# Kernel tuning notes

Measured on AMD Instinct MI355X. Metric: run time of the kernel, lower is better.

Reference implementation:

```python
import jax, jax.numpy as jnp
import numpy as np

EPS_MSG = 1e-7
EPS_BN = 1e-5


def _seg_softmax(logits, seg, num_segments):
    # logits: [E, D] per-edge logits; softmax over edges sharing the same dst node
    m = jax.ops.segment_max(logits, seg, num_segments=num_segments)
    m = jnp.where(jnp.isfinite(m), m, 0.0)
    e = jnp.exp(logits - m[seg])
    s = jax.ops.segment_sum(e, seg, num_segments=num_segments)
    return e / (s[seg] + 1e-16)


def _batchnorm(h, gamma, beta):
    mu = jnp.mean(h, axis=0)
    var = jnp.var(h, axis=0)
    return (h - mu) * jax.lax.rsqrt(var + EPS_BN) * gamma + beta


def setup_inputs() -> dict:
    key = jax.random.key(0)
    ks = jax.random.split(key, 12)
    N, E, G, D, L = 100000, 600000, 512, 128, 7
    x = jax.random.randint(ks[0], (N, 9), 0, 64, dtype=jnp.int32)
    edge_index = jax.random.randint(ks[1], (2, E), 0, N, dtype=jnp.int32)
    edge_attr = jax.random.randint(ks[2], (E, 3), 0, 8, dtype=jnp.int32)
    batch = jnp.sort(jax.random.randint(ks[3], (N,), 0, G, dtype=jnp.int32))
    rf_pred = jax.random.uniform(ks[4], (G,), dtype=jnp.float32)
    atom_emb = jax.random.normal(ks[5], (9, 64, D), dtype=jnp.float32) * 0.02
    bond_emb = jax.random.normal(ks[6], (3, 8, D), dtype=jnp.float32) * 0.02
    conv_w = jax.random.normal(ks[7], (L, D, D), dtype=jnp.float32) * 0.02
    conv_b = jnp.zeros((L, D), dtype=jnp.float32)
    ts = jnp.ones((L,), dtype=jnp.float32)  # learnable inverse temperatures (init 1/t style)
    gammas = jnp.ones((L, D), dtype=jnp.float32)
    bn_betas = jnp.zeros((L, D), dtype=jnp.float32)
    final_w = jax.random.normal(ks[8], (D, 1), dtype=jnp.float32) * 0.02
    final_b = jnp.zeros((1,), dtype=jnp.float32)
    beta = jnp.array([0.5], dtype=jnp.float32)
    return {"x": x, "edge_index": edge_index, "edge_attr": edge_attr, "batch": batch,
            "rf_pred": rf_pred, "atom_emb": atom_emb, "bond_emb": bond_emb,
            "conv_w": conv_w, "conv_b": conv_b, "ts": ts, "gammas": gammas,
            "bn_betas": bn_betas, "final_w": final_w, "final_b": final_b, "beta": beta}


def reference(x, edge_index, edge_attr, batch, rf_pred, atom_emb, bond_emb,
              conv_w, conv_b, ts, gammas, bn_betas, final_w, final_b, beta):
    N = x.shape[0]
    G = rf_pred.shape[0]
    L = conv_w.shape[0]
    src, dst = edge_index[0], edge_index[1]

    # AtomEncoder / BondEncoder: sum of per-feature embeddings
    h = jax.vmap(lambda tab, idx: tab[idx], in_axes=(0, 1))(atom_emb, x).sum(0)          # [N, D]
    e_emb = jax.vmap(lambda tab, idx: tab[idx], in_axes=(0, 1))(bond_emb, edge_attr).sum(0)  # [E, D]

    def genconv(l, hin):
        msg = jax.nn.relu(hin[src] + e_emb) + EPS_MSG          # [E, D]
        alpha = _seg_softmax(msg * ts[l], dst, N)              # softmax aggregation weights
        aggr = jax.ops.segment_sum(alpha * msg, dst, num_segments=N)  # [N, D]
        return (hin + aggr) @ conv_w[l] + conv_b[l]

    # res+ DeeperGCN
    h = genconv(0, h)
    for l in range(1, L):
        h2 = jax.nn.relu(_batchnorm(h, gammas[l - 1], bn_betas[l - 1]))
        h = genconv(l, h2) + h
    h = jax.nn.relu(_batchnorm(h, gammas[L - 1], bn_betas[L - 1]))

    # mean graph pooling
    counts = jnp.maximum(jax.ops.segment_sum(jnp.ones((N,), h.dtype), batch, num_segments=G), 1.0)
    hg = jax.ops.segment_sum(h, batch, num_segments=G) / counts[:, None]  # [G, D]

    dgcn_pred = hg @ final_w + final_b  # [G, 1]
    return (1.0 - beta) * jax.nn.sigmoid(dgcn_pred) + beta * rf_pred.reshape(-1, 1)
```

## Files before the change

### kernel.cpp

```cpp
#include <hip/hip_runtime.h>
#include <hip/hip_fp16.h>
#include <math.h>

#define D 128
#define PF 8

typedef _Float16 f16x8 __attribute__((ext_vector_type(8)));
typedef float f32x4_t __attribute__((ext_vector_type(4)));


__global__ void hist_kernel(const int* __restrict__ edge_index, int* __restrict__ deg, int E) {
    int e = blockIdx.x * blockDim.x + threadIdx.x;
    if (e >= E) return;
    atomicAdd(&deg[edge_index[E + e]], 1);
}

__global__ void scanA_kernel(const int* __restrict__ deg, int* __restrict__ bsum, int n) {
    __shared__ int red[256];
    int b = blockIdx.x, t = threadIdx.x;
    int base = b * 1024 + t * 4;
    int s = 0;
#pragma unroll
    for (int j = 0; j < 4; ++j)
        if (base + j < n) s += deg[base + j];
    red[t] = s;
    __syncthreads();
    for (int off = 128; off > 0; off >>= 1) {
        if (t < off) red[t] += red[t + off];
        __syncthreads();
    }
    if (t == 0) bsum[b] = red[0];
}

__global__ void scanB_kernel(int* __restrict__ bsum, int nb) {
    __shared__ int sh[256];
    int t = threadIdx.x;
    sh[t] = (t < nb) ? bsum[t] : 0;
    __syncthreads();
    for (int off = 1; off < 256; off <<= 1) {
        int v = (t >= off) ? sh[t - off] : 0;
        __syncthreads();
        sh[t] += v;
        __syncthreads();
    }
    if (t < nb) bsum[t] = (t == 0) ? 0 : sh[t - 1];
}

__global__ void scanC_kernel(const int* __restrict__ deg, const int* __restrict__ boff,
                             int* __restrict__ row_start, int n) {
    __shared__ int sh[256];
    int b = blockIdx.x, t = threadIdx.x;
    int base = b * 1024 + t * 4;
    int v[4];
#pragma unroll
    for (int j = 0; j < 4; ++j) v[j] = (base + j < n) ? deg[base + j] : 0;
    int p[4];
    p[0] = 0; p[1] = v[0]; p[2] = v[0] + v[1]; p[3] = v[0] + v[1] + v[2];
    int s = p[3] + v[3];
    sh[t] = s;
    __syncthreads();
    for (int off = 1; off < 256; off <<= 1) {
        int x = (t >= off) ? sh[t - off] : 0;
        __syncthreads();
        sh[t] += x;
        __syncthreads();
    }
    int off0 = boff[b] + sh[t] - s;
#pragma unroll
    for (int j = 0; j < 4; ++j)
        if (base + j < n) row_start[base + j] = off0 + p[j];
    if (base <= n - 1 && n - 1 < base + 4) row_start[n] = off0 + s;
}

__global__ void scatter_kernel(const int* __restrict__ edge_index, const int* __restrict__ edge_attr,
                               int* __restrict__ cursor, int2* __restrict__ csr, int E) {
    int e = blockIdx.x * blockDim.x + threadIdx.x;
    if (e >= E) return;
    int src = edge_index[e];
    int dst = edge_index[E + e];
    int pos = atomicAdd(&cursor[dst], 1);
    int a0 = edge_attr[e * 3], a1 = edge_attr[e * 3 + 1], a2 = edge_attr[e * 3 + 2];
    csr[pos] = make_int2(src, a0 | (a1 << 3) | (a2 << 6));
}

__global__ void ev_build_kernel(const float* __restrict__ bond_emb, __half2* __restrict__ evt) {
    int idx = blockIdx.x * blockDim.x + threadIdx.x;
    if (idx >= 512 * 64) return;
    int combo = idx >> 6, j = idx & 63;
    int d0 = 2 * j;
    float ex = bond_emb[(combo & 7) * D + d0] +
               bond_emb[(8 + ((combo >> 3) & 7)) * D + d0] +
               bond_emb[(16 + ((combo >> 6) & 7)) * D + d0];
    float ey = bond_emb[(combo & 7) * D + d0 + 1] +
               bond_emb[(8 + ((combo >> 3) & 7)) * D + d0 + 1] +
               bond_emb[(16 + ((combo >> 6) & 7)) * D + d0 + 1];
    evt[idx] = __floats2half2_rn(ex, ey);
}

__global__ void wt_build_kernel(const float* __restrict__ conv_w, _Float16* __restrict__ wt,
                                int total) {
    int idx = blockIdx.x * blockDim.x + threadIdx.x;
    if (idx >= total) return;
    int l = idx >> 14;
    int rem = idx & 16383;
    int n = rem >> 7, k = rem & 127;
    wt[idx] = (_Float16)conv_w[(l << 14) + k * 128 + n];
}

__global__ void gstart_kernel(const int* __restrict__ batch, int* __restrict__ gstart,
                              int N, int G) {
    int n = blockIdx.x * blockDim.x + threadIdx.x;
    if (n >= N) return;
    if (n == 0) {
        for (int g = 0; g <= batch[0]; ++g) gstart[g] = 0;
    } else {
        int b0 = batch[n - 1], b1 = batch[n];
        for (int g = b0 + 1; g <= b1; ++g) gstart[g] = n;
    }
    if (n == N - 1) {
        for (int g = batch[N - 1] + 1; g <= G; ++g) gstart[g] = N;
    }
}


__global__ void atom_embed_kernel(const int* __restrict__ x,
                                  const float* __restrict__ atom_emb,
                                  float* __restrict__ h, _Float16* __restrict__ h16, int N) {
    long long idx = (long long)blockIdx.x * blockDim.x + threadIdx.x;
    if (idx >= (long long)N * D) return;
    int n = (int)(idx >> 7);
    int d = (int)(idx & 127);
    float acc = 0.f;
#pragma unroll
    for (int f = 0; f < 9; ++f) {
        int v = x[n * 9 + f];
        acc += atom_emb[(long long)(f * 64 + v) * D + d];
    }
    h[idx] = acc;
    h16[idx] = (_Float16)acc;
}

__global__ void bn_reduce_finalize_kernel(const float* __restrict__ partial, int nb,
                                          const float* __restrict__ gamma,
                                          const float* __restrict__ bnbeta, float invN,
                                          float* __restrict__ aArr, float* __restrict__ bArr) {
    __shared__ float r1[256], r2[256];
    int d = blockIdx.x, t = threadIdx.x;
    float a1 = 0.f, a2 = 0.f;
    for (int i = t; i < nb; i += 256) {
        a1 += partial[(long long)i * 256 + d];
        a2 += partial[(long long)i * 256 + 128 + d];
    }
    r1[t] = a1; r2[t] = a2;
    __syncthreads();
    for (int off = 128; off > 0; off >>= 1) {
        if (t < off) { r1[t] += r1[t + off]; r2[t] += r2[t + off]; }
        __syncthreads();
    }
    if (t == 0) {
        float mean = r1[0] * invN;
        float var = r2[0] * invN - mean * mean;
        float a = rsqrtf(var + 1e-5f) * gamma[d];
        aArr[d] = a;
        bArr[d] = bnbeta[d] - mean * a;
    }
}

__global__ __launch_bounds__(256, 8) void fused_layer_kernel(
        const __half2* __restrict__ h16c, const float* __restrict__ h,
        const float* __restrict__ aArr, const float* __restrict__ bArr, int applyBN,
        const float* __restrict__ ts, int l,
        const int* __restrict__ row_start, const int2* __restrict__ csr,
        const __half2* __restrict__ evt,
        const _Float16* __restrict__ wt, const float* __restrict__ bias,
        int residual, float* __restrict__ hout, _Float16* __restrict__ h16out,
        float* __restrict__ partial, int N) {
    __shared__ __align__(16) char smem[8704];
    _Float16* yh = (_Float16*)smem;
    __half2* tile = (__half2*)smem;

    int t = threadIdx.x;
    int row0 = blockIdx.x * 32;
    int wave = t >> 6;
    int lane = t & 63;
    float tsl = ts[l];
    int a = row0 + wave * 8;

    float2 bnA = make_float2(1.f, 0.f), bnB = make_float2(0.f, 0.f);
    if (applyBN) {
        bnA = ((const float2*)aArr)[lane];
        bnB = ((const float2*)bArr)[lane];
    }

    int rsv = row_start[min(a + min(lane, 8), N)];
    int s0 = __builtin_amdgcn_readlane(rsv, 0);
    int s1 = __builtin_amdgcn_readlane(rsv, 8);

#pragma unroll
    for (int i = 0; i < 8; ++i) {
        int r = a + i;
        float2 hs = make_float2(0.f, 0.f);
        if (r < N) {
            hs = __half22float2(h16c[(size_t)r * 64 + lane]);
            if (applyBN) {
                hs.x = fmaxf(hs.x * bnA.x + bnB.x, 0.f);
                hs.y = fmaxf(hs.y * bnA.y + bnB.y, 0.f);
            }
        }
        tile[(wave * 8 + i) * 68 + lane] = __floats2half2_rn(hs.x, hs.y);
    }

    int c0 = s0;
    int2 ea = make_int2(0, 0);
    if (c0 + lane < s1) ea = csr[c0 + lane];

    __half2 hvS[PF], evS[PF];
#pragma unroll
    for (int k = 0; k < PF; ++k) {
        int pp = s0 + k;
        if (pp < s1) {
            int q = pp - c0;
            int srcp = __builtin_amdgcn_readlane(ea.x, q);
            int cbp = __builtin_amdgcn_readlane(ea.y, q);
            hvS[k] = h16c[(size_t)srcp * 64 + lane];
            evS[k] = evt[(size_t)cbp * 64 + lane];
        }
    }

    int cur = 0;
    int nend = __builtin_amdgcn_readlane(rsv, min(cur + 1, 8));
    while (cur < 8 && nend == s0) {
        cur++;
        nend = __builtin_amdgcn_readlane(rsv, min(cur + 1, 8));
    }

    float accwx = 0.f, accwy = 0.f, accmx = 0.f, accmy = 0.f;
    int total = s1 - s0;
    for (int it = 0; it < total; it += PF) {
#pragma unroll
        for (int k = 0; k < PF; ++k) {
            int p = s0 + it + k;
            if (p < s1) {
                float2 hv = __half22float2(hvS[k]);
                float2 ev = __half22float2(evS[k]);
                if (applyBN) {
                    hv.x = fmaxf(hv.x * bnA.x + bnB.x, 0.f);
                    hv.y = fmaxf(hv.y * bnA.y + bnB.y, 0.f);
                }
                float mx = fmaxf(hv.x + ev.x, 0.f) + 1e-7f;
                float my = fmaxf(hv.y + ev.y, 0.f) + 1e-7f;
                float wx = __expf(mx * tsl);
                float wy = __expf(my * tsl);
                accwx += wx; accmx += wx * mx;
                accwy += wy; accmy += wy * my;
                int pp = p + PF;
                if (pp < s1) {
                    if (pp >= c0 + 64) {
                        c0 += 64;
                        ea = (c0 + lane < s1) ? csr[c0 + lane] : make_int2(0, 0);
                    }
                    int q = pp - c0;
                    int srcp = __builtin_amdgcn_readlane(ea.x, q);
                    int cbp = __builtin_amdgcn_readlane(ea.y, q);
                    hvS[k] = h16c[(size_t)srcp * 64 + lane];
                    evS[k] = evt[(size_t)cbp * 64 + lane];
                }
                while (cur < 8 && nend == p + 1) {
                    int slot = (wave * 8 + cur) * 68 + lane;
                    float2 y = __half22float2(tile[slot]);
                    y.x += accmx / (accwx + 1e-16f);
                    y.y += accmy / (accwy + 1e-16f);
                    tile[slot] = __floats2half2_rn(y.x, y.y);
                    accwx = accwy = accmx = accmy = 0.f;
                    cur++;
                    nend = __builtin_amdgcn_readlane(rsv, min(cur + 1, 8));
                }
            }
        }
    }
    __syncthreads();

    int ln = t & 15;
    int quad = (t & 63) >> 4;
    int rt = wave >> 1;
    int ctb = (wave & 1) * 4;

    float cs[4] = {0.f, 0.f, 0.f, 0.f};
    float cq[4] = {0.f, 0.f, 0.f, 0.f};
    const _Float16* ap = yh + (rt * 16 + ln) * 136 + quad * 8;
#pragma unroll
    for (int ct = 0; ct < 4; ++ct) {
        int ctg = ctb + ct;
        int colg = ctg * 16 + ln;
        const _Float16* bp = wt + (size_t)colg * 128 + quad * 8;
        f32x4_t c = {0.f, 0.f, 0.f, 0.f};
#pragma unroll
        for (int kk = 0; kk < 4; ++kk) {
            f16x8 av = *(const f16x8*)(ap + kk * 32);
            f16x8 bv = *(const f16x8*)(bp + kk * 32);
            c = __builtin_amdgcn_mfma_f32_16x16x32_f16(av, bv, c, 0, 0, 0);
        }
        float bsv = bias[colg];
#pragma unroll
        for (int reg = 0; reg < 4; ++reg) {
            int r = row0 + rt * 16 + quad * 4 + reg;
            if (r < N) {
                long long off = (long long)r * D + colg;
                float o = c[reg] + bsv;
                if (residual) o += h[off];
                hout[off] = o;
                h16out[off] = (_Float16)o;
                cs[ct] += o; cq[ct] += o * o;
            }
        }
    }

    __syncthreads();
    float* stats = (float*)smem;
    int grp = rt * 4 + quad;
#pragma unroll
    for (int ct = 0; ct < 4; ++ct) {
        int colg = (ctb + ct) * 16 + ln;
        stats[grp * 256 + colg] = cs[ct];
        stats[grp * 256 + 128 + colg] = cq[ct];
    }
    __syncthreads();
    float ssum = 0.f;
#pragma unroll
    for (int g = 0; g < 8; ++g) ssum += stats[g * 256 + t];
    partial[(long long)blockIdx.x * 256 + t] = ssum;
}

__global__ void pool_head_kernel(const float* __restrict__ h, const float* __restrict__ aArr,
                                 const float* __restrict__ bArr, const int* __restrict__ gstart,
                                 const float* __restrict__ fw, const float* __restrict__ fb,
                                 const float* __restrict__ beta, const float* __restrict__ rf,
                                 float* __restrict__ out) {
    __shared__ float red[256];
    int g = blockIdx.x, t = threadIdx.x;
    int d = t & 127, half = t >> 7;
    int s0 = gstart[g], s1 = gstart[g + 1];
    float a = aArr[d], b = bArr[d];
    float acc = 0.f;
    for (int n = s0 + half; n < s1; n += 2)
        acc += fmaxf(h[(long long)n * D + d] * a + b, 0.f);
    red[t] = acc;
    __syncthreads();
    if (t < 128) red[t] += red[t + 128];
    __syncthreads();
    if (t < 64) {
        float v = red[t] * fw[t] + red[t + 64] * fw[t + 64];
#pragma unroll
        for (int off = 32; off > 0; off >>= 1) v += __shfl_down(v, off);
        if (t == 0) {
            float c = fmaxf((float)(s1 - s0), 1.f);
            float pred = v / c + fb[0];
            float sig = 1.f / (1.f + __expf(-pred));
            float bb = beta[0];
            out[g] = (1.f - bb) * sig + bb * rf[g];
        }
    }
}

static inline size_t align16(size_t x) { return (x + 15) & ~(size_t)15; }

extern "C" void kernel_launch(void* const* d_in, const int* in_sizes, int n_in,
                              void* d_out, int out_size, void* d_ws, size_t ws_size,
                              hipStream_t stream) {
    const int* x = (const int*)d_in[0];
    const int* edge_index = (const int*)d_in[1];
    const int* edge_attr = (const int*)d_in[2];
    const int* batch = (const int*)d_in[3];
    const float* rf_pred = (const float*)d_in[4];
    const float* atom_emb = (const float*)d_in[5];
    const float* bond_emb = (const float*)d_in[6];
    const float* conv_w = (const float*)d_in[7];
    const float* conv_b = (const float*)d_in[8];
    const float* ts = (const float*)d_in[9];
    const float* gammas = (const float*)d_in[10];
    const float* bn_betas = (const float*)d_in[11];
    const float* final_w = (const float*)d_in[12];
    const float* final_b = (const float*)d_in[13];
    const float* beta = (const float*)d_in[14];
    float* out = (float*)d_out;

    int N = in_sizes[0] / 9;
    int E = in_sizes[1] / 2;
    int G = in_sizes[4];
    int L = in_sizes[9];

    int mmBlocks = (N + 31) / 32;
    size_t ND = (size_t)N * D;

    char* p = (char*)d_ws;
    float* h_a = (float*)p;          p += align16(ND * 4);
    float* h_b = (float*)p;          p += align16(ND * 4);
    _Float16* h16_a = (_Float16*)p;  p += align16(ND * 2);
    _Float16* h16_b = (_Float16*)p;  p += align16(ND * 2);
    __half2* evt = (__half2*)p;      p += align16((size_t)512 * 64 * 4);
    _Float16* wt = (_Float16*)p;     p += align16((size_t)L * 16384 * 2);
    float* partial = (float*)p;      p += align16((size_t)256 * mmBlocks * 4);
    float* aArr = (float*)p;         p += align16((size_t)D * 4);
    float* bArr = (float*)p;         p += align16((size_t)D * 4);
    int* gstart = (int*)p;           p += align16((size_t)(G + 1) * 4);
    int* deg = (int*)p;              p += align16((size_t)N * 4);
    int* row_start = (int*)p;        p += align16((size_t)(N + 1) * 4);
    int* cursor = (int*)p;           p += align16((size_t)N * 4);
    int* bsum = (int*)p;             p += align16((size_t)256 * 4);
    int2* csr = (int2*)p;            p += align16((size_t)E * 8);

    long long ndThreads = (long long)N * D;
    int ndBlocks = (int)((ndThreads + 255) / 256);
    int eBlocks = (E + 255) / 256;
    int nBlocks = (N + 255) / 256;
    int nb1024 = (N + 1023) / 1024;
    int wtTotal = L * 16384;
    float invN = 1.0f / (float)N;

    hipMemsetAsync(deg, 0, (size_t)N * sizeof(int), stream);
    hist_kernel<<<eBlocks, 256, 0, stream>>>(edge_index, deg, E);
    scanA_kernel<<<nb1024, 256, 0, stream>>>(deg, bsum, N);
    scanB_kernel<<<1, 256, 0, stream>>>(bsum, nb1024);
    scanC_kernel<<<nb1024, 256, 0, stream>>>(deg, bsum, row_start, N);
    hipMemcpyAsync(cursor, row_start, (size_t)N * sizeof(int), hipMemcpyDeviceToDevice, stream);
    scatter_kernel<<<eBlocks, 256, 0, stream>>>(edge_index, edge_attr, cursor, csr, E);
    ev_build_kernel<<<(512 * 64 + 255) / 256, 256, 0, stream>>>(bond_emb, evt);
    wt_build_kernel<<<(wtTotal + 255) / 256, 256, 0, stream>>>(conv_w, wt, wtTotal);
    gstart_kernel<<<nBlocks, 256, 0, stream>>>(batch, gstart, N, G);

    atom_embed_kernel<<<ndBlocks, 256, 0, stream>>>(x, atom_emb, h_a, h16_a, N);

    float* hc = h_a;
    float* hn = h_b;
    _Float16* h16c = h16_a;
    _Float16* h16n = h16_b;
    for (int l = 0; l < L; ++l) {
        int applyBN = (l >= 1) ? 1 : 0;
        if (applyBN) {
            bn_reduce_finalize_kernel<<<128, 256, 0, stream>>>(
                partial, mmBlocks, gammas + (size_t)(l - 1) * D,
                bn_betas + (size_t)(l - 1) * D, invN, aArr, bArr);
        }
        fused_layer_kernel<<<mmBlocks, 256, 0, stream>>>(
            (const __half2*)h16c, hc, aArr, bArr, applyBN, ts, l, row_start, csr, evt,
            wt + (size_t)l * 16384, conv_b + (size_t)l * D,
            applyBN, hn, h16n, partial, N);
        float* tmp = hc; hc = hn; hn = tmp;
        _Float16* tmp16 = h16c; h16c = h16n; h16n = tmp16;
    }

    bn_reduce_finalize_kernel<<<128, 256, 0, stream>>>(
        partial, mmBlocks, gammas + (size_t)(L - 1) * D,
        bn_betas + (size_t)(L - 1) * D, invN, aArr, bArr);
    pool_head_kernel<<<G, 256, 0, stream>>>(hc, aArr, bArr, gstart,
                                            final_w, final_b, beta, rf_pred, out);
}
```

Baseline: 924.8 us.

## Drop fp32 hidden state, keep fp16 only, and halve rows per layer block

Removes the fp32 copy of the node features entirely. The residual add in the fused layer kernel and the final pooling now read the fp16 buffer, and the atom embedding writes only fp16. This cuts the per-layer global memory traffic of reading and writing a full fp32 N×128 tensor. The fused layer kernel also moves to 128-thread blocks covering 16 rows, which doubles the grid, and the stats reduction is adjusted to match. The cost is that the residual stream is now accumulated in half precision across layers, which may add numerical error.

```diff
diff --git a/kernel.cpp b/kernel.cpp
--- a/kernel.cpp
+++ b/kernel.cpp
@@ -125,7 +125,7 @@
 
 __global__ void atom_embed_kernel(const int* __restrict__ x,
                                   const float* __restrict__ atom_emb,
-                                  float* __restrict__ h, _Float16* __restrict__ h16, int N) {
+                                  _Float16* __restrict__ h16, int N) {
     long long idx = (long long)blockIdx.x * blockDim.x + threadIdx.x;
     if (idx >= (long long)N * D) return;
     int n = (int)(idx >> 7);
@@ -136,7 +136,6 @@
         int v = x[n * 9 + f];
         acc += atom_emb[(long long)(f * 64 + v) * D + d];
     }
-    h[idx] = acc;
     h16[idx] = (_Float16)acc;
 }
 
@@ -166,21 +165,21 @@
     }
 }
 
-__global__ __launch_bounds__(256, 8) void fused_layer_kernel(
-        const __half2* __restrict__ h16c, const float* __restrict__ h,
+__global__ __launch_bounds__(128, 8) void fused_layer_kernel(
+        const __half2* __restrict__ h16c,
         const float* __restrict__ aArr, const float* __restrict__ bArr, int applyBN,
         const float* __restrict__ ts, int l,
         const int* __restrict__ row_start, const int2* __restrict__ csr,
         const __half2* __restrict__ evt,
         const _Float16* __restrict__ wt, const float* __restrict__ bias,
-        int residual, float* __restrict__ hout, _Float16* __restrict__ h16out,
+        int residual, _Float16* __restrict__ h16out,
         float* __restrict__ partial, int N) {
-    __shared__ __align__(16) char smem[8704];
+    __shared__ __align__(16) char smem[8192];
     _Float16* yh = (_Float16*)smem;
     __half2* tile = (__half2*)smem;
 
     int t = threadIdx.x;
-    int row0 = blockIdx.x * 32;
+    int row0 = blockIdx.x * 16;
     int wave = t >> 6;
     int lane = t & 63;
     float tsl = ts[l];
@@ -282,16 +281,14 @@
 
     int ln = t & 15;
     int quad = (t & 63) >> 4;
-    int rt = wave >> 1;
-    int ctb = (wave & 1) * 4;
+    const _Float16* h16in = (const _Float16*)h16c;
 
     float cs[4] = {0.f, 0.f, 0.f, 0.f};
     float cq[4] = {0.f, 0.f, 0.f, 0.f};
-    const _Float16* ap = yh + (rt * 16 + ln) * 136 + quad * 8;
+    const _Float16* ap = yh + ln * 136 + quad * 8;
 #pragma unroll
     for (int ct = 0; ct < 4; ++ct) {
-        int ctg = ctb + ct;
-        int colg = ctg * 16 + ln;
+        int colg = (wave * 4 + ct) * 16 + ln;
         const _Float16* bp = wt + (size_t)colg * 128 + quad * 8;
         f32x4_t c = {0.f, 0.f, 0.f, 0.f};
 #pragma unroll
@@ -303,12 +300,11 @@
         float bsv = bias[colg];
 #pragma unroll
         for (int reg = 0; reg < 4; ++reg) {
-            int r = row0 + rt * 16 + quad * 4 + reg;
+            int r = row0 + quad * 4 + reg;
             if (r < N) {
                 long long off = (long long)r * D + colg;
                 float o = c[reg] + bsv;
-                if (residual) o += h[off];
-                hout[off] = o;
+                if (residual) o += (float)h16in[off];
                 h16out[off] = (_Float16)o;
                 cs[ct] += o; cq[ct] += o * o;
             }
@@ -317,21 +313,25 @@
 
     __syncthreads();
     float* stats = (float*)smem;
-    int grp = rt * 4 + quad;
+    int grp = wave * 4 + quad;
 #pragma unroll
     for (int ct = 0; ct < 4; ++ct) {
-        int colg = (ctb + ct) * 16 + ln;
+        int colg = (wave * 4 + ct) * 16 + ln;
         stats[grp * 256 + colg] = cs[ct];
         stats[grp * 256 + 128 + colg] = cq[ct];
     }
     __syncthreads();
-    float ssum = 0.f;
-#pragma unroll
-    for (int g = 0; g < 8; ++g) ssum += stats[g * 256 + t];
-    partial[(long long)blockIdx.x * 256 + t] = ssum;
-}
-
-__global__ void pool_head_kernel(const float* __restrict__ h, const float* __restrict__ aArr,
+    float ssumA = 0.f, ssumB = 0.f;
+#pragma unroll
+    for (int g = 0; g < 8; ++g) {
+        ssumA += stats[g * 256 + t];
+        ssumB += stats[g * 256 + 128 + t];
+    }
+    partial[(long long)blockIdx.x * 256 + t] = ssumA;
+    partial[(long long)blockIdx.x * 256 + 128 + t] = ssumB;
+}
+
+__global__ void pool_head_kernel(const _Float16* __restrict__ h16, const float* __restrict__ aArr,
                                  const float* __restrict__ bArr, const int* __restrict__ gstart,
                                  const float* __restrict__ fw, const float* __restrict__ fb,
                                  const float* __restrict__ beta, const float* __restrict__ rf,
@@ -343,7 +343,7 @@
     float a = aArr[d], b = bArr[d];
     float acc = 0.f;
     for (int n = s0 + half; n < s1; n += 2)
-        acc += fmaxf(h[(long long)n * D + d] * a + b, 0.f);
+        acc += fmaxf((float)h16[(long long)n * D + d] * a + b, 0.f);
     red[t] = acc;
     __syncthreads();
     if (t < 128) red[t] += red[t + 128];
@@ -389,12 +389,10 @@
     int G = in_sizes[4];
     int L = in_sizes[9];
 
-    int mmBlocks = (N + 31) / 32;
+    int mmBlocks = (N + 15) / 16;
     size_t ND = (size_t)N * D;
 
     char* p = (char*)d_ws;
-    float* h_a = (float*)p;          p += align16(ND * 4);
-    float* h_b = (float*)p;          p += align16(ND * 4);
     _Float16* h16_a = (_Float16*)p;  p += align16(ND * 2);
     _Float16* h16_b = (_Float16*)p;  p += align16(ND * 2);
     __half2* evt = (__half2*)p;      p += align16((size_t)512 * 64 * 4);
@@ -428,10 +426,8 @@
     wt_build_kernel<<<(wtTotal + 255) / 256, 256, 0, stream>>>(conv_w, wt, wtTotal);
     gstart_kernel<<<nBlocks, 256, 0, stream>>>(batch, gstart, N, G);
 
-    atom_embed_kernel<<<ndBlocks, 256, 0, stream>>>(x, atom_emb, h_a, h16_a, N);
-
-    float* hc = h_a;
-    float* hn = h_b;
+    atom_embed_kernel<<<ndBlocks, 256, 0, stream>>>(x, atom_emb, h16_a, N);
+
     _Float16* h16c = h16_a;
     _Float16* h16n = h16_b;
     for (int l = 0; l < L; ++l) {
@@ -441,17 +437,16 @@
                 partial, mmBlocks, gammas + (size_t)(l - 1) * D,
                 bn_betas + (size_t)(l - 1) * D, invN, aArr, bArr);
         }
-        fused_layer_kernel<<<mmBlocks, 256, 0, stream>>>(
-            (const __half2*)h16c, hc, aArr, bArr, applyBN, ts, l, row_start, csr, evt,
+        fused_layer_kernel<<<mmBlocks, 128, 0, stream>>>(
+            (const __half2*)h16c, aArr, bArr, applyBN, ts, l, row_start, csr, evt,
             wt + (size_t)l * 16384, conv_b + (size_t)l * D,
-            applyBN, hn, h16n, partial, N);
-        float* tmp = hc; hc = hn; hn = tmp;
+            applyBN, h16n, partial, N);
         _Float16* tmp16 = h16c; h16c = h16n; h16n = tmp16;
     }
 
     bn_reduce_finalize_kernel<<<128, 256, 0, stream>>>(
         partial, mmBlocks, gammas + (size_t)(L - 1) * D,
         bn_betas + (size_t)(L - 1) * D, invN, aArr, bArr);
-    pool_head_kernel<<<G, 256, 0, stream>>>(hc, aArr, bArr, gstart,
+    pool_head_kernel<<<G, 256, 0, stream>>>(h16c, aArr, bArr, gstart,
                                             final_w, final_b, beta, rf_pred, out);
 }
```

Result: no change. 917.8 us (-0.8%).
